# Kernel tuning notes

Measured on AMD Instinct MI355X. Metric: run time of the kernel, lower is better.

## Reference

```python
import jax, jax.numpy as jnp
import numpy as np

NUM_LEAVES = 256
EPS = 1e-6
SHARPNESS = 1.0   # init_sharpness, non-trainable buffer
BIAS_SHIFT = -2.0


def _generalized_gcd(w1, w2, lambd):
    # lambd: per-node bias -> andness via sigmoid; broadcast over batch
    lam = jax.nn.sigmoid(lambd)
    a = jnp.abs(w1) + EPS
    b = jnp.abs(w2) + EPS
    return lam * jnp.minimum(a, b) + (1.0 - lam) * jnp.maximum(a, b)


def setup_inputs() -> dict:
    key = jax.random.key(0)
    ks = jax.random.split(key, 6)
    B, L = 65536, NUM_LEAVES
    x = jax.random.normal(ks[0], (B, L), jnp.float32)
    # xavier-like scale for the leaf projection
    W_leaf = jax.random.normal(ks[1], (L, L), jnp.float32) * (1.0 / np.sqrt(L))
    weights = jax.random.uniform(ks[2], (L - 1, 2), jnp.float32, 0.5, 1.5)
    biases = jax.random.uniform(ks[3], (L - 1,), jnp.float32) * 0.1
    w_out = jax.random.normal(ks[4], (1, 1), jnp.float32)
    b_out = jnp.full((1,), 0.5, jnp.float32)
    return {"x": x, "W_leaf": W_leaf, "weights": weights,
            "biases": biases, "w_out": w_out, "b_out": b_out}


def reference(x, W_leaf, weights, biases, w_out, b_out):
    # InputToLeafFC: sigmoid(sharpness * (x @ W^T + bias_shift))
    leaf = jax.nn.sigmoid(SHARPNESS * (x @ W_leaf.T + BIAS_SHIFT))  # (B, L)

    # The original pops two nodes from the front of the queue and appends the
    # result; for a power-of-two leaf count this is exactly a level-by-level
    # pairwise tree reduction, with node weights consumed in order.
    cur = leaf
    off = 0
    n = cur.shape[1]
    while n > 1:  # log2(L) levels, each fully vectorized over (batch, pairs)
        m = n // 2
        w = weights[off:off + m]   # (m, 2)
        b = biases[off:off + m]    # (m,)
        left = cur[:, 0::2] * w[:, 0]
        right = cur[:, 1::2] * w[:, 1]
        cur = _generalized_gcd(left, right, b)  # (B, m)
        off += m
        n = m
    # fc_out: Linear(1,1) then sigmoid -> (B, 1)
    return jax.nn.sigmoid(cur * w_out[0, 0] + b_out[0])
```

## Files before the change

kernel.cpp:

```cpp
#include <hip/hip_runtime.h>
#include <stdint.h>


#define EPS 1e-6f
#define LOG2E 1.44269504088896340736f
#define PARAM_OFF 131072

typedef __attribute__((ext_vector_type(8))) short short8;
typedef __attribute__((ext_vector_type(4))) short short4_t;
typedef __attribute__((ext_vector_type(4))) float float4_t;

__device__ __forceinline__ float fast_sigmoid(float z) {
    float e = __builtin_amdgcn_exp2f(-z * LOG2E);
    return __builtin_amdgcn_rcpf(1.0f + e);
}

__device__ __forceinline__ short f2bf(float f) {
    uint32_t u = __builtin_bit_cast(uint32_t, f);
    u += 0x7FFFu + ((u >> 16) & 1u);
    return (short)(u >> 16);
}

__device__ __forceinline__ short8 pack8(float4 a, float4 b) {
    short8 s;
    s[0] = f2bf(a.x); s[1] = f2bf(a.y); s[2] = f2bf(a.z); s[3] = f2bf(a.w);
    s[4] = f2bf(b.x); s[5] = f2bf(b.y); s[6] = f2bf(b.z); s[7] = f2bf(b.w);
    return s;
}

__device__ __forceinline__ float ggcd(float l, float r, float lam) {
    float a = fabsf(l) + EPS;
    float b = fabsf(r) + EPS;
    float mn = fminf(a, b);
    float mx = fmaxf(a, b);
    return fmaf(lam, mn - mx, mx);
}

__device__ __forceinline__ void lds16(const void* g, void* l) {
    __builtin_amdgcn_global_load_lds(
        (const __attribute__((address_space(1))) unsigned int*)g,
        (__attribute__((address_space(3))) unsigned int*)l, 16, 0, 0);
}

__device__ __forceinline__ void tree_reduce(float4_t acc[16], int c0,
                                            const float4* pv, float res[4]) {
    #pragma unroll
    for (int t = 0; t < 16; ++t) {
        #pragma unroll
        for (int r = 0; r < 4; ++r) acc[t][r] = fast_sigmoid(acc[t][r] - 2.0f);
    }
    #pragma unroll
    for (int tp = 0; tp < 8; ++tp) {
        float4 p = pv[c0 * 8 + tp];
        #pragma unroll
        for (int r = 0; r < 4; ++r)
            acc[tp][r] = ggcd(acc[2*tp][r] * p.x, acc[2*tp+1][r] * p.y, p.z);
    }
    #pragma unroll
    for (int tp = 0; tp < 4; ++tp) {
        float4 p = pv[128 + c0 * 4 + tp];
        #pragma unroll
        for (int r = 0; r < 4; ++r)
            acc[tp][r] = ggcd(acc[2*tp][r] * p.x, acc[2*tp+1][r] * p.y, p.z);
    }
    #pragma unroll
    for (int tp = 0; tp < 2; ++tp) {
        float4 p = pv[192 + c0 * 2 + tp];
        #pragma unroll
        for (int r = 0; r < 4; ++r)
            acc[tp][r] = ggcd(acc[2*tp][r] * p.x, acc[2*tp+1][r] * p.y, p.z);
    }
    {
        float4 p = pv[224 + c0];
        #pragma unroll
        for (int r = 0; r < 4; ++r)
            res[r] = ggcd(acc[0][r] * p.x, acc[1][r] * p.y, p.z);
    }
}

__global__ __launch_bounds__(256)
void convert_w(const float* __restrict__ Wl, const float* __restrict__ wts,
               const float* __restrict__ bia, char* __restrict__ img) {
    int i = blockIdx.x * 256 + threadIdx.x;
    int a = i * 8;
    int kt   = a >> 15;
    int s    = a & 32767;
    int j    = s >> 7;
    int b    = s & 127;
    int cpos = b >> 4;
    int h    = (b >> 3) & 1;
    int c    = cpos ^ (j & 7);
    int k    = kt * 64 + c * 8 + h * 4;
    int src  = ((j & 15) << 4) | (j >> 4);
    float4 w4 = *(const float4*)&Wl[src * 256 + k];
    short4_t s4;
    s4.x = f2bf(w4.x); s4.y = f2bf(w4.y); s4.z = f2bf(w4.z); s4.w = f2bf(w4.w);
    *(short4_t*)&img[a] = s4;

    if (i < 255) {
        float4* pv = (float4*)(img + PARAM_OFF);
        pv[i] = make_float4(wts[2 * i], wts[2 * i + 1], fast_sigmoid(bia[i]), 0.f);
    } else if (i == 255) {
        ((float4*)(img + PARAM_OFF))[255] = make_float4(0.f, 0.f, 0.f, 0.f);
    }
}

__global__ __launch_bounds__(512, 4)
void btln_main(const float* __restrict__ x, const char* __restrict__ img,
               const float* __restrict__ wout, const float* __restrict__ bout,
               float* __restrict__ out) {
    __shared__ short Wt[2][16384];
    __shared__ float4 pv[256];

    const int tid  = threadIdx.x;
    const int lane = tid & 63;
    const int wv   = tid >> 6;
    const int c0   = lane & 15;
    const int q    = lane >> 4;

    if (tid < 256) pv[tid] = ((const float4*)(img + PARAM_OFF))[tid];

    const char* gW = img + wv * 4096 + lane * 16;
    {
        char* l = (char*)&Wt[0][wv * 2048];
        #pragma unroll
        for (int it = 0; it < 4; ++it)
            lds16(gW + it * 1024, l + it * 1024);
    }

    const int rowbase = blockIdx.x * 128 + wv * 16;
    const float* xr = x + (size_t)(rowbase + c0) * 256;

    short8 af[4][2];
    {
        float4 p0, p1, p2, p3, q0, q1, q2, q3;
        p0 = *(const float4*)(xr + q * 8);
        p1 = *(const float4*)(xr + q * 8 + 4);
        p2 = *(const float4*)(xr + 32 + q * 8);
        p3 = *(const float4*)(xr + 32 + q * 8 + 4);
        q0 = *(const float4*)(xr + 64 + q * 8);
        q1 = *(const float4*)(xr + 64 + q * 8 + 4);
        q2 = *(const float4*)(xr + 96 + q * 8);
        q3 = *(const float4*)(xr + 96 + q * 8 + 4);
        af[0][0] = pack8(p0, p1); af[0][1] = pack8(p2, p3);
        __builtin_amdgcn_sched_barrier(0);
        p0 = *(const float4*)(xr + 128 + q * 8);
        p1 = *(const float4*)(xr + 128 + q * 8 + 4);
        p2 = *(const float4*)(xr + 160 + q * 8);
        p3 = *(const float4*)(xr + 160 + q * 8 + 4);
        af[1][0] = pack8(q0, q1); af[1][1] = pack8(q2, q3);
        __builtin_amdgcn_sched_barrier(0);
        q0 = *(const float4*)(xr + 192 + q * 8);
        q1 = *(const float4*)(xr + 192 + q * 8 + 4);
        q2 = *(const float4*)(xr + 224 + q * 8);
        q3 = *(const float4*)(xr + 224 + q * 8 + 4);
        af[2][0] = pack8(p0, p1); af[2][1] = pack8(p2, p3);
        __builtin_amdgcn_sched_barrier(0);
        af[3][0] = pack8(q0, q1); af[3][1] = pack8(q2, q3);
    }

    float4_t acc[16];
    #pragma unroll
    for (int t = 0; t < 16; ++t) acc[t] = (float4_t){0.f, 0.f, 0.f, 0.f};

    __syncthreads();

    const int vx = c0 & 7;

#define KSTEP(kt, LAST)                                                       \
    {                                                                         \
        const short* cur = Wt[(kt) & 1];                                      \
        if (!(LAST)) {                                                        \
            char* l = (char*)&Wt[((kt) + 1) & 1][wv * 2048];                  \
            const char* g = gW + ((kt) + 1) * 32768;                          \
            lds16(g, l);                                                      \
            lds16(g + 1024, l + 1024);                                        \
            lds16(g + 2048, l + 2048);                                        \
            lds16(g + 3072, l + 3072);                                        \
        }                                                                     \
        _Pragma("unroll")                                                     \
        for (int t = 0; t < 16; ++t) {                                        \
            const short* base = &cur[(t * 16 + c0) * 64];                     \
            short8 bf0 = *(const short8*)&base[(q ^ vx) * 8];                 \
            short8 bf1 = *(const short8*)&base[((q + 4) ^ vx) * 8];           \
            acc[t] = __builtin_amdgcn_mfma_f32_16x16x32_bf16(                 \
                af[kt][0], bf0, acc[t], 0, 0, 0);                             \
            acc[t] = __builtin_amdgcn_mfma_f32_16x16x32_bf16(                 \
                af[kt][1], bf1, acc[t], 0, 0, 0);                             \
        }                                                                     \
        if (!(LAST)) __syncthreads();                                         \
    }

    KSTEP(0, 0)
    KSTEP(1, 0)
    KSTEP(2, 0)
    KSTEP(3, 1)
#undef KSTEP

    float res[4];
    tree_reduce(acc, c0, pv, res);

    const int offs[4] = {240, 248, 252, 254};
    #pragma unroll
    for (int k = 0; k < 4; ++k) {
        float4 p = pv[offs[k] + (c0 >> (k + 1))];
        bool isLeft = ((c0 >> k) & 1) == 0;
        #pragma unroll
        for (int r = 0; r < 4; ++r) {
            float other = __shfl_xor(res[r], 1 << k, 64);
            float lf = isLeft ? res[r] : other;
            float rt = isLeft ? other  : res[r];
            res[r] = ggcd(lf * p.x, rt * p.y, p.z);
        }
    }

    if (c0 == 0) {
        const float wo = wout[0];
        const float bo = bout[0];
        #pragma unroll
        for (int r = 0; r < 4; ++r)
            out[rowbase + q * 4 + r] = fast_sigmoid(fmaf(res[r], wo, bo));
    }
}

extern "C" void kernel_launch(void* const* d_in, const int* in_sizes, int n_in,
                              void* d_out, int out_size, void* d_ws, size_t ws_size,
                              hipStream_t stream) {
    const float* x   = (const float*)d_in[0];
    const float* Wl  = (const float*)d_in[1];
    const float* wts = (const float*)d_in[2];
    const float* bia = (const float*)d_in[3];
    const float* wo  = (const float*)d_in[4];
    const float* bo  = (const float*)d_in[5];
    float* out = (float*)d_out;
    char* img = (char*)d_ws;

    convert_w<<<dim3(64), dim3(256), 0, stream>>>(Wl, wts, bia, img);

    const int rows = out_size;
    dim3 grid(rows / 128), block(512);
    btln_main<<<grid, block, 0, stream>>>(x, img, wo, bo, out);
}
```

Before: 118.1 us.

## Fuse weight conversion into main kernel and stream x per k-step

```diff
diff --git a/kernel.cpp b/kernel.cpp
--- a/kernel.cpp
+++ b/kernel.cpp
@@ -4,7 +4,6 @@
 
 #define EPS 1e-6f
 #define LOG2E 1.44269504088896340736f
-#define PARAM_OFF 131072
 
 typedef __attribute__((ext_vector_type(8))) short short8;
 typedef __attribute__((ext_vector_type(4))) short short4_t;
@@ -36,10 +35,24 @@
     return fmaf(lam, mn - mx, mx);
 }
 
-__device__ __forceinline__ void lds16(const void* g, void* l) {
-    __builtin_amdgcn_global_load_lds(
-        (const __attribute__((address_space(1))) unsigned int*)g,
-        (__attribute__((address_space(3))) unsigned int*)l, 16, 0, 0);
+__device__ __forceinline__ void stage_tile(const float* __restrict__ Wl,
+                                           short* dst, int kt, int tid) {
+    const int m  = tid & 15;
+    const int g  = (tid >> 4) & 3;
+    const int jb = tid >> 4;
+    const int cpos2h = (m + 4 * g) & 15;
+    const int cpos = cpos2h >> 1;
+    const int h    = cpos2h & 1;
+    #pragma unroll
+    for (int i = 0; i < 8; ++i) {
+        int j   = i * 32 + jb;
+        int col = kt * 64 + ((cpos ^ (j & 7)) << 3) + h * 4;
+        int src = ((j & 15) << 4) | (j >> 4);
+        float4 w4 = *(const float4*)&Wl[src * 256 + col];
+        short4_t s4;
+        s4.x = f2bf(w4.x); s4.y = f2bf(w4.y); s4.z = f2bf(w4.z); s4.w = f2bf(w4.w);
+        *(short4_t*)((char*)dst + j * 128 + cpos2h * 8) = s4;
+    }
 }
 
 __device__ __forceinline__ void tree_reduce(float4_t acc[16], int c0,
@@ -78,35 +91,9 @@
     }
 }
 
-__global__ __launch_bounds__(256)
-void convert_w(const float* __restrict__ Wl, const float* __restrict__ wts,
-               const float* __restrict__ bia, char* __restrict__ img) {
-    int i = blockIdx.x * 256 + threadIdx.x;
-    int a = i * 8;
-    int kt   = a >> 15;
-    int s    = a & 32767;
-    int j    = s >> 7;
-    int b    = s & 127;
-    int cpos = b >> 4;
-    int h    = (b >> 3) & 1;
-    int c    = cpos ^ (j & 7);
-    int k    = kt * 64 + c * 8 + h * 4;
-    int src  = ((j & 15) << 4) | (j >> 4);
-    float4 w4 = *(const float4*)&Wl[src * 256 + k];
-    short4_t s4;
-    s4.x = f2bf(w4.x); s4.y = f2bf(w4.y); s4.z = f2bf(w4.z); s4.w = f2bf(w4.w);
-    *(short4_t*)&img[a] = s4;
-
-    if (i < 255) {
-        float4* pv = (float4*)(img + PARAM_OFF);
-        pv[i] = make_float4(wts[2 * i], wts[2 * i + 1], fast_sigmoid(bia[i]), 0.f);
-    } else if (i == 255) {
-        ((float4*)(img + PARAM_OFF))[255] = make_float4(0.f, 0.f, 0.f, 0.f);
-    }
-}
-
 __global__ __launch_bounds__(512, 4)
-void btln_main(const float* __restrict__ x, const char* __restrict__ img,
+void btln_main(const float* __restrict__ x, const float* __restrict__ Wl,
+               const float* __restrict__ wts, const float* __restrict__ bia,
                const float* __restrict__ wout, const float* __restrict__ bout,
                float* __restrict__ out) {
     __shared__ short Wt[2][16384];
@@ -118,46 +105,24 @@
     const int c0   = lane & 15;
     const int q    = lane >> 4;
 
-    if (tid < 256) pv[tid] = ((const float4*)(img + PARAM_OFF))[tid];
-
-    const char* gW = img + wv * 4096 + lane * 16;
-    {
-        char* l = (char*)&Wt[0][wv * 2048];
-        #pragma unroll
-        for (int it = 0; it < 4; ++it)
-            lds16(gW + it * 1024, l + it * 1024);
-    }
+    if (tid < 255) {
+        pv[tid] = make_float4(wts[2 * tid], wts[2 * tid + 1],
+                              fast_sigmoid(bia[tid]), 0.f);
+    } else if (tid == 255) {
+        pv[255] = make_float4(0.f, 0.f, 0.f, 0.f);
+    }
+
+    stage_tile(Wl, Wt[0], 0, tid);
 
     const int rowbase = blockIdx.x * 128 + wv * 16;
     const float* xr = x + (size_t)(rowbase + c0) * 256;
 
-    short8 af[4][2];
-    {
-        float4 p0, p1, p2, p3, q0, q1, q2, q3;
-        p0 = *(const float4*)(xr + q * 8);
-        p1 = *(const float4*)(xr + q * 8 + 4);
-        p2 = *(const float4*)(xr + 32 + q * 8);
-        p3 = *(const float4*)(xr + 32 + q * 8 + 4);
-        q0 = *(const float4*)(xr + 64 + q * 8);
-        q1 = *(const float4*)(xr + 64 + q * 8 + 4);
-        q2 = *(const float4*)(xr + 96 + q * 8);
-        q3 = *(const float4*)(xr + 96 + q * 8 + 4);
-        af[0][0] = pack8(p0, p1); af[0][1] = pack8(p2, p3);
-        __builtin_amdgcn_sched_barrier(0);
-        p0 = *(const float4*)(xr + 128 + q * 8);
-        p1 = *(const float4*)(xr + 128 + q * 8 + 4);
-        p2 = *(const float4*)(xr + 160 + q * 8);
-        p3 = *(const float4*)(xr + 160 + q * 8 + 4);
-        af[1][0] = pack8(q0, q1); af[1][1] = pack8(q2, q3);
-        __builtin_amdgcn_sched_barrier(0);
-        q0 = *(const float4*)(xr + 192 + q * 8);
-        q1 = *(const float4*)(xr + 192 + q * 8 + 4);
-        q2 = *(const float4*)(xr + 224 + q * 8);
-        q3 = *(const float4*)(xr + 224 + q * 8 + 4);
-        af[2][0] = pack8(p0, p1); af[2][1] = pack8(p2, p3);
-        __builtin_amdgcn_sched_barrier(0);
-        af[3][0] = pack8(q0, q1); af[3][1] = pack8(q2, q3);
-    }
+    float4 r0 = *(const float4*)(xr + q * 8);
+    float4 r1 = *(const float4*)(xr + q * 8 + 4);
+    float4 r2 = *(const float4*)(xr + 32 + q * 8);
+    float4 r3 = *(const float4*)(xr + 32 + q * 8 + 4);
+    short8 afc0 = pack8(r0, r1);
+    short8 afc1 = pack8(r2, r3);
 
     float4_t acc[16];
     #pragma unroll
@@ -170,13 +135,13 @@
 #define KSTEP(kt, LAST)                                                       \
     {                                                                         \
         const short* cur = Wt[(kt) & 1];                                      \
-        if (!(LAST)) {                                                        \
-            char* l = (char*)&Wt[((kt) + 1) & 1][wv * 2048];                  \
-            const char* g = gW + ((kt) + 1) * 32768;                          \
-            lds16(g, l);                                                      \
-            lds16(g + 1024, l + 1024);                                        \
-            lds16(g + 2048, l + 2048);                                        \
-            lds16(g + 3072, l + 3072);                                        \
+        float4 n0, n1, n2, n3;                                                \
+        if (!(LAST)) {                          \
+            const float* xn = xr + ((kt) + 1) * 64;                           \
+            n0 = *(const float4*)(xn + q * 8);                                \
+            n1 = *(const float4*)(xn + q * 8 + 4);                            \
+            n2 = *(const float4*)(xn + 32 + q * 8);                           \
+            n3 = *(const float4*)(xn + 32 + q * 8 + 4);                       \
         }                                                                     \
         _Pragma("unroll")                                                     \
         for (int t = 0; t < 16; ++t) {                                        \
@@ -184,11 +149,17 @@
             short8 bf0 = *(const short8*)&base[(q ^ vx) * 8];                 \
             short8 bf1 = *(const short8*)&base[((q + 4) ^ vx) * 8];           \
             acc[t] = __builtin_amdgcn_mfma_f32_16x16x32_bf16(                 \
-                af[kt][0], bf0, acc[t], 0, 0, 0);                             \
+                afc0, bf0, acc[t], 0, 0, 0);                                  \
             acc[t] = __builtin_amdgcn_mfma_f32_16x16x32_bf16(                 \
-                af[kt][1], bf1, acc[t], 0, 0, 0);                             \
+                afc1, bf1, acc[t], 0, 0, 0);                                  \
         }                                                                     \
-        if (!(LAST)) __syncthreads();                                         \
+        __builtin_amdgcn_sched_barrier(0);        \
+        if (!(LAST)) {                                                        \
+            stage_tile(Wl, Wt[((kt) + 1) & 1], (kt) + 1, tid);                \
+            afc0 = pack8(n0, n1);                                             \
+            afc1 = pack8(n2, n3);                                             \
+            __syncthreads();                         \
+        }                                                                     \
     }
 
     KSTEP(0, 0)
@@ -233,11 +204,8 @@
     const float* wo  = (const float*)d_in[4];
     const float* bo  = (const float*)d_in[5];
     float* out = (float*)d_out;
-    char* img = (char*)d_ws;
-
-    convert_w<<<dim3(64), dim3(256), 0, stream>>>(Wl, wts, bia, img);
 
     const int rows = out_size;
     dim3 grid(rows / 128), block(512);
-    btln_main<<<grid, block, 0, stream>>>(x, img, wo, bo, out);
-}
+    btln_main<<<grid, block, 0, stream>>>(x, Wl, wts, bia, wo, bo, out);
+}
```

Result: slower. 121.1 us (+2.5%).
